# Performance work log

Measured on AMD Instinct MI355X. Metric: run time of the kernel, lower is better.

## Reference

```python
import jax, jax.numpy as jnp
import numpy as np

# --- obs layout constants (from source) ---
OBS_TERM_DIMS = (3, 3, 3, 3, 29, 29, 29, 96)
HISTORY_LEN = 5
BASE_LIN_VEL_DIM = 3
_OFFS = [0]
for d in OBS_TERM_DIMS[:-1]:
    _OFFS.append(_OFFS[-1] + d * HISTORY_LEN)

N = 131072

def _extract_frame(x, frame_idx):
    # proprio frame: 7 terms, 99 dims total
    parts = []
    for t in range(7):
        d = OBS_TERM_DIMS[t]
        s = _OFFS[t] + frame_idx * d
        parts.append(x[:, s:s + d])
    return jnp.concatenate(parts, axis=-1)

def _extract_elevation(x):
    s = _OFFS[7] + (HISTORY_LEN - 1) * OBS_TERM_DIMS[7]
    return x[:, s:s + OBS_TERM_DIMS[7]]  # [N,96]

def setup_inputs() -> dict:
    key = jax.random.key(0)
    ks = jax.random.split(key, 16)
    s = 0.05
    return {
        "x": jax.random.normal(ks[0], (N, 975), jnp.float32),
        "vae_W1": jax.random.normal(ks[1], (480, 256), jnp.float32) * s,
        "vae_b1": jnp.zeros((256,), jnp.float32),
        "vae_Wz": jax.random.normal(ks[2], (256, 32), jnp.float32) * s,
        "vae_bz": jnp.zeros((32,), jnp.float32),
        "vae_Wv": jax.random.normal(ks[3], (256, 3), jnp.float32) * s,
        "vae_bv": jnp.zeros((3,), jnp.float32),
        "ae_W1": jax.random.normal(ks[4], (96, 64), jnp.float32) * s,
        "ae_b1": jnp.zeros((64,), jnp.float32),
        "ae_W2": jax.random.normal(ks[5], (64, 32), jnp.float32) * s,
        "ae_b2": jnp.zeros((32,), jnp.float32),
        "gate_W1": jax.random.normal(ks[6], (32, 64), jnp.float32) * s,
        "gate_b1": jnp.zeros((64,), jnp.float32),
        "gate_W2": jax.random.normal(ks[7], (64, 5), jnp.float32) * s,
        "gate_b2": jnp.zeros((5,), jnp.float32),
        "eW1": jax.random.normal(ks[8], (5, 166, 128), jnp.float32) * s,
        "eb1": jnp.zeros((5, 128), jnp.float32),
        "eW2": jax.random.normal(ks[9], (5, 128, 128), jnp.float32) * s,
        "eb2": jnp.zeros((5, 128), jnp.float32),
        "eW3": jax.random.normal(ks[10], (5, 128, 29), jnp.float32) * s,
        "eb3": jnp.zeros((5, 29), jnp.float32),
    }

def reference(x, vae_W1, vae_b1, vae_Wz, vae_bz, vae_Wv, vae_bv,
              ae_W1, ae_b1, ae_W2, ae_b2,
              gate_W1, gate_b1, gate_W2, gate_b2,
              eW1, eb1, eW2, eb2, eW3, eb3):
    elu = jax.nn.elu
    # feature extraction
    o_t = _extract_frame(x, HISTORY_LEN - 1)                       # [N,99]
    frames = [_extract_frame(x, i)[:, BASE_LIN_VEL_DIM:] for i in range(HISTORY_LEN)]
    vae_hist = jnp.concatenate(frames, axis=-1)                    # [N,480]
    e_t = _extract_elevation(x)                                    # [N,96]
    # VAE estimator (no_grad in original)
    h = elu(vae_hist @ vae_W1 + vae_b1)
    z_H = jax.lax.stop_gradient(h @ vae_Wz + vae_bz)               # [N,32]
    v_pred = jax.lax.stop_gradient(h @ vae_Wv + vae_bv)            # [N,3]
    # AE estimator (no_grad)
    ha = elu(e_t @ ae_W1 + ae_b1)
    z_E = jax.lax.stop_gradient(ha @ ae_W2 + ae_b2)                # [N,32]
    # experts: batched GEMM over 5 experts
    inp = jnp.concatenate([o_t, v_pred, z_H, z_E], axis=-1)        # [N,166]
    h1 = elu(jnp.einsum('ni,eih->neh', inp, eW1) + eb1)            # [N,5,128]
    h2 = elu(jnp.einsum('neh,ehk->nek', h1, eW2) + eb2)            # [N,5,128]
    acts = jnp.einsum('neh,ehk->nek', h2, eW3) + eb3               # [N,5,29]
    # gating
    gl = elu(z_E @ gate_W1 + gate_b1) @ gate_W2 + gate_b2          # [N,5]
    w = jax.nn.softmax(gl, axis=-1)
    return jnp.einsum('ne,nek->nk', w, acts)                       # [N,29]
```

## Files before the change

### kernel.cpp

```cpp
#include <hip/hip_runtime.h>
#include <math.h>

typedef _Float16 f16;
typedef f16  f16x8 __attribute__((ext_vector_type(8)));
typedef float f32x4 __attribute__((ext_vector_type(4)));
typedef unsigned short ushort_t;

#define MFMA16(a, b, c) __builtin_amdgcn_mfma_f32_16x16x32_f16((a), (b), (c), 0, 0, 0)

#define W1T_E 0
#define WZV_E 131072
#define A1T_E 143360
#define A2T_E 149504
#define G1T_E 151552
#define G2T_E 153600
#define E1T_E 154624
#define E2T_E 277504
#define E3T_E 359424
#define F32_B 759808

#define S2_OFF   0
#define B0_OFF   36864
#define H2_OFF   17408
#define ELEV_OFF 62528
#define HA_OFF   62528
#define ZE_OFF   71744
#define WF_OFF   75840
#define SMEM_SZ  77888

__device__ __forceinline__ float elu_f(float v) {
    float e = __expf(v) - 1.f;
    return v > 0.f ? v : e;
}

__device__ __forceinline__ unsigned pk(float a, float b) {
    ushort_t u0 = __builtin_bit_cast(ushort_t, (f16)a);
    ushort_t u1 = __builtin_bit_cast(ushort_t, (f16)b);
    return (unsigned)u0 | ((unsigned)u1 << 16);
}

__device__ __forceinline__ void store4(f16* p, f32x4 v) {
    uint2 t; t.x = pk(v[0], v[1]); t.y = pk(v[2], v[3]);
    *(uint2*)p = t;
}

__device__ __forceinline__ void elu_store4(f16* p, f32x4 v) {
    uint2 t; t.x = pk(elu_f(v[0]), elu_f(v[1])); t.y = pk(elu_f(v[2]), elu_f(v[3]));
    *(uint2*)p = t;
}

__device__ __forceinline__ void sync_lds() {
    asm volatile("s_waitcnt lgkmcnt(0)" ::: "memory");
    __builtin_amdgcn_s_barrier();
    asm volatile("" ::: "memory");
    __builtin_amdgcn_sched_barrier(0);
}

__global__ void prep_kernel(const float* __restrict__ vW1, const float* __restrict__ vWz,
                            const float* __restrict__ vWv, const float* __restrict__ aW1,
                            const float* __restrict__ aW2, const float* __restrict__ gW1,
                            const float* __restrict__ gW2, const float* __restrict__ eW1,
                            const float* __restrict__ eW2, const float* __restrict__ eW3,
                            const float* __restrict__ vbz, const float* __restrict__ vbv,
                            const float* __restrict__ eb3, const float* __restrict__ gb2,
                            char* __restrict__ ws)
{
    int i = blockIdx.x * 256 + threadIdx.x;
    f16* H = (f16*)ws;
    if (i < 131072) {
        int c = i >> 9, ks = i & 511;
        int xcol = 12 + ks;
        float v = 0.f;
        if (xcol >= 15 && xcol <= 494) {
            int hc;
            if (xcol < 60) {
                int t = xcol / 15; int rm = xcol - 15 * t; int f = rm / 3;
                hc = 96 * f + 3 * (t - 1) + (rm - 3 * f);
            } else {
                int t2 = (xcol - 60) / 145; int rm = xcol - 60 - 145 * t2; int f = rm / 29;
                hc = 96 * f + 9 + 29 * t2 + (rm - 29 * f);
            }
            v = vW1[hc * 256 + c];
        }
        H[i] = (f16)v;
    } else if (i < 143360) {
        int j = i - 131072; int c = j / 256, k = j - c * 256;
        float v = (c < 32) ? vWz[k * 32 + c] : ((c < 35) ? vWv[k * 3 + (c - 32)] : 0.f);
        H[i] = (f16)v;
    } else if (i < 149504) {
        int j = i - 143360; int c = j / 96, k = j - c * 96;
        H[i] = (f16)aW1[k * 64 + c];
    } else if (i < 151552) {
        int j = i - 149504; int c = j / 64, k = j - c * 64;
        H[i] = (f16)aW2[k * 32 + c];
    } else if (i < 153600) {
        int j = i - 151552; int c = j / 32, k = j - c * 32;
        H[i] = (f16)gW1[k * 64 + c];
    } else if (i < 154624) {
        int j = i - 153600; int c = j / 64, k = j - c * 64;
        H[i] = (f16)((c < 5) ? gW2[k * 5 + c] : 0.f);
    } else if (i < 277504) {
        int j = i - 154624; int e = j / 24576, jj = j - e * 24576;
        int c = jj / 192, k = jj - c * 192;
        int ko = (k >= 5 && k < 107)   ? (k - 5)
               : (k >= 108 && k < 140) ? (k - 6)
               : (k >= 144 && k < 176) ? (k - 10) : -1;
        H[i] = (f16)((ko >= 0) ? eW1[(e * 166 + ko) * 128 + c] : 0.f);
    } else if (i < 359424) {
        int j = i - 277504; int e = j / 16384, jj = j - e * 16384;
        int c = jj / 128, k = jj - c * 128;
        H[i] = (f16)eW2[(e * 128 + k) * 128 + c];
    } else if (i < 379904) {
        int j = i - 359424; int e = j / 4096, jj = j - e * 4096;
        int c = jj / 128, k = jj - c * 128;
        H[i] = (f16)((c < 29) ? eW3[(e * 128 + k) * 29 + c] : 0.f);
    } else if (i < 380128) {
        int j = i - 379904;
        float* F = (float*)(ws + F32_B);
        float v;
        if (j < 48)       v = (j < 32) ? vbz[j] : ((j < 35) ? vbv[j - 32] : 0.f);
        else if (j < 208) { int t = j - 48; int e = t >> 5, c = t & 31;
                            v = (c < 29) ? eb3[e * 29 + c] : 0.f; }
        else              { int t = j - 208; v = (t < 5) ? gb2[t] : 0.f; }
        F[j] = v;
    }
}

__global__ __launch_bounds__(512, 4) void moe_fused(
    const float* __restrict__ x,
    const float* __restrict__ vb1,
    const float* __restrict__ ab1,
    const float* __restrict__ ab2,
    const float* __restrict__ gb1,
    const float* __restrict__ eb1,
    const float* __restrict__ eb2,
    const char* __restrict__ ws,
    float* __restrict__ out)
{
    __shared__ __align__(16) char smem[SMEM_SZ];
    const int tid  = threadIdx.x;
    const int wv   = tid >> 6;
    const int lane = tid & 63;
    const int lr   = lane & 15;
    const int lg   = lane >> 4;
    const int wh   = wv & 1;
    const int wc   = wv >> 1;
    const int row0 = (int)blockIdx.x * 64;

    const f16* W1T = (const f16*)ws + W1T_E;
    const f16* WZV = (const f16*)ws + WZV_E;
    const f16* A1T = (const f16*)ws + A1T_E;
    const f16* A2T = (const f16*)ws + A2T_E;
    const f16* G1T = (const f16*)ws + G1T_E;
    const f16* G2T = (const f16*)ws + G2T_E;
    const f16* E1T = (const f16*)ws + E1T_E;
    const f16* E2T = (const f16*)ws + E2T_E;
    const f16* E3T = (const f16*)ws + E3T_E;
    const float* BZV  = (const float*)(ws + F32_B);
    const float* EB3P = BZV + 48;
    const float* GB2P = BZV + 208;

    f16* sS2 = (f16*)(smem + S2_OFF);
    f16* sEl = (f16*)(smem + ELEV_OFF);
    f16* sHA = (f16*)(smem + HA_OFF);
    f16* sZE = (f16*)(smem + ZE_OFF);
    f16* sH  = (f16*)(smem + S2_OFF);
    f16* sB0 = (f16*)(smem + B0_OFF);
    f16* sH1 = (f16*)(smem + S2_OFF);
    f16* sH2 = (f16*)(smem + H2_OFF);
    float* sWf = (float*)(smem + WF_OFF);

    {
        if (tid < 16) *(unsigned*)(smem + 62464 + 4 * tid) = 0u;
        const int sr0 = wv * 8;
        for (int rr = 0; rr < 8; ++rr) {
            const int r = sr0 + rr;
            const float* xr = x + (size_t)(row0 + r) * 975;
            if (lane < 48) {
                float a = xr[879 + 2 * lane], b = xr[880 + 2 * lane];
                *(unsigned*)(sEl + r * 104 + 2 * lane) = pk(a, b);
            }
            f16* dst = sS2 + r * 488;
#pragma unroll
            for (int j = 0; j < 4; ++j) {
                int p = j * 64 + lane;
                if (p < 244) {
                    float a = 0.f, b = 0.f;
                    if (p < 242) { a = xr[12 + 2 * p]; b = xr[13 + 2 * p]; }
                    *(unsigned*)(dst + 2 * p) = pk(a, b);
                }
            }
        }
    }
    sync_lds();

    f32x4 g3acc[2];
    {
        f32x4 bi = *(const f32x4*)(ab1 + 16 * wc + 4 * lg);
        g3acc[0] = bi; g3acc[1] = bi;
#pragma unroll
        for (int ks = 0; ks < 3; ++ks) {
            f16x8 wf = *(const f16x8*)(A1T + (16 * wc + lr) * 96 + 32 * ks + 8 * lg);
#pragma unroll
            for (int mm = 0; mm < 2; ++mm) {
                int m = 2 * wh + mm;
                f16x8 bf = *(const f16x8*)(sEl + (16 * m + lr) * 104 + 32 * ks + 8 * lg);
                g3acc[mm] = MFMA16(wf, bf, g3acc[mm]);
            }
        }
    }
    sync_lds();
#pragma unroll
    for (int mm = 0; mm < 2; ++mm)
        elu_store4(sHA + (16 * (2 * wh + mm) + lr) * 72 + 16 * wc + 4 * lg, g3acc[mm]);
    sync_lds();

    if (wv < 4) {
        int c = wv >> 1, h = wv & 1;
        f32x4 bi = *(const f32x4*)(ab2 + 16 * c + 4 * lg);
        f32x4 acc[2]; acc[0] = bi; acc[1] = bi;
#pragma unroll
        for (int ks = 0; ks < 2; ++ks) {
            f16x8 wf = *(const f16x8*)(A2T + (16 * c + lr) * 64 + 32 * ks + 8 * lg);
#pragma unroll
            for (int mm = 0; mm < 2; ++mm) {
                int m = 2 * h + mm;
                f16x8 bf = *(const f16x8*)(sHA + (16 * m + lr) * 72 + 32 * ks + 8 * lg);
                acc[mm] = MFMA16(wf, bf, acc[mm]);
            }
        }
#pragma unroll
        for (int mm = 0; mm < 2; ++mm)
            store4(sZE + (16 * (2 * h + mm) + lr) * 32 + 16 * c + 4 * lg, acc[mm]);
    }
    sync_lds();

    {
        f32x4 bi = *(const f32x4*)(gb1 + 16 * wc + 4 * lg);
        f32x4 acc[2]; acc[0] = bi; acc[1] = bi;
        f16x8 wf = *(const f16x8*)(G1T + (16 * wc + lr) * 32 + 8 * lg);
#pragma unroll
        for (int mm = 0; mm < 2; ++mm) {
            int m = 2 * wh + mm;
            f16x8 bf = *(const f16x8*)(sZE + (16 * m + lr) * 32 + 8 * lg);
            acc[mm] = MFMA16(wf, bf, acc[mm]);
        }
#pragma unroll
        for (int mm = 0; mm < 2; ++mm)
            elu_store4(sHA + (16 * (2 * wh + mm) + lr) * 72 + 16 * wc + 4 * lg, acc[mm]);
    }
    sync_lds();

    if (wv == 0) {
        f32x4 bi = *(const f32x4*)(GB2P + 4 * lg);
        f32x4 acc[4];
#pragma unroll
        for (int m = 0; m < 4; ++m) acc[m] = bi;
#pragma unroll
        for (int ks = 0; ks < 2; ++ks) {
            f16x8 wf = *(const f16x8*)(G2T + lr * 64 + 32 * ks + 8 * lg);
#pragma unroll
            for (int m = 0; m < 4; ++m) {
                f16x8 bf = *(const f16x8*)(sHA + (16 * m + lr) * 72 + 32 * ks + 8 * lg);
                acc[m] = MFMA16(wf, bf, acc[m]);
            }
        }
        if (lg == 0) {
#pragma unroll
            for (int m = 0; m < 4; ++m)
                *(f32x4*)(sWf + (16 * m + lr) * 8) = acc[m];
        } else if (lg == 1) {
#pragma unroll
            for (int m = 0; m < 4; ++m)
                sWf[(16 * m + lr) * 8 + 4] = acc[m][0];
        }
    }
    sync_lds();

    if (tid < 64) {
        float g[5];
#pragma unroll
        for (int e = 0; e < 5; ++e) g[e] = sWf[tid * 8 + e];
        float mx = fmaxf(fmaxf(fmaxf(g[0], g[1]), fmaxf(g[2], g[3])), g[4]);
        float s = 0.f;
#pragma unroll
        for (int e = 0; e < 5; ++e) { g[e] = __expf(g[e] - mx); s += g[e]; }
        float inv = 1.f / s;
#pragma unroll
        for (int e = 0; e < 5; ++e) sWf[tid * 8 + e] = g[e] * inv;
    }

    f32x4 acc1[4][2];
#pragma unroll
    for (int nt = 0; nt < 2; ++nt) {
        f32x4 bi = *(const f32x4*)(vb1 + 32 * wv + 16 * nt + 4 * lg);
#pragma unroll
        for (int m = 0; m < 4; ++m) acc1[m][nt] = bi;
    }
    __builtin_amdgcn_s_setprio(1);
#pragma unroll
    for (int ks = 0; ks < 16; ++ks) {
        f16x8 wf[2];
#pragma unroll
        for (int nt = 0; nt < 2; ++nt)
            wf[nt] = *(const f16x8*)(W1T + (32 * wv + 16 * nt + lr) * 512 + 32 * ks + 8 * lg);
#pragma unroll
        for (int m = 0; m < 4; ++m) {
            f16x8 bf = *(const f16x8*)(sS2 + (16 * m + lr) * 488 + 32 * ks + 8 * lg);
#pragma unroll
            for (int nt = 0; nt < 2; ++nt)
                acc1[m][nt] = MFMA16(wf[nt], bf, acc1[m][nt]);
        }
    }
    __builtin_amdgcn_s_setprio(0);
    const int r_ot = tid >> 3, sub = tid & 7;
    ushort_t otv[13];
#pragma unroll
    for (int i = 0; i < 13; ++i) {
        int j = sub + 8 * i;
        if (j < 99) {
            int s;
            if (j < 3) s = j;
            else if (j < 12) { int jj = j - 3; int t = jj / 3;
                               s = 15 * (t + 1) + (jj - 3 * t); }
            else { int jj = j - 12; int t2 = jj / 29;
                   s = 164 + 145 * t2 + (jj - 29 * t2); }
            otv[i] = __builtin_bit_cast(ushort_t, sS2[r_ot * 488 + s]);
        }
    }
    float we5[5];
    sync_lds();

#pragma unroll
    for (int m = 0; m < 4; ++m)
#pragma unroll
        for (int nt = 0; nt < 2; ++nt)
            elu_store4(sH + (16 * m + lr) * 264 + 32 * wv + 16 * nt + 4 * lg, acc1[m][nt]);
#pragma unroll
    for (int i = 0; i < 13; ++i) {
        int j = sub + 8 * i;
        if (j < 99) sB0[r_ot * 200 + 5 + j] = __builtin_bit_cast(f16, otv[i]);
    }
    {
        char* b0r = (char*)sB0 + r_ot * 400;
        if (sub == 0) { *(uint2*)(b0r + 0) = (uint2){0u, 0u}; *(ushort_t*)(b0r + 8) = 0; }
        else if (sub == 1) { *(uint2*)(b0r + 280) = (uint2){0u, 0u}; }
        else if (sub == 2) { *(uint4*)(b0r + 352) = (uint4){0u,0u,0u,0u}; }
        else if (sub == 3) { *(uint4*)(b0r + 368) = (uint4){0u,0u,0u,0u}; }
    }
    {
        int r = tid >> 3, c4 = tid & 7;
        uint2 v = *(uint2*)((char*)sZE + r * 64 + 8 * c4);
        *(uint2*)((char*)sB0 + r * 400 + 288 + 8 * c4) = v;
    }
#pragma unroll
    for (int e = 0; e < 5; ++e) we5[e] = sWf[(16 * (wv & 3) + lr) * 8 + e];
    sync_lds();

    if (wv < 6) {
        int c = wv >> 1, h = wv & 1;
        f32x4 bz = *(const f32x4*)(BZV + 16 * c + 4 * lg);
        f32x4 acc[2]; acc[0] = bz; acc[1] = bz;
#pragma unroll
        for (int ks = 0; ks < 8; ++ks) {
            f16x8 wf = *(const f16x8*)(WZV + (16 * c + lr) * 256 + 32 * ks + 8 * lg);
#pragma unroll
            for (int mm = 0; mm < 2; ++mm) {
                int m = 2 * h + mm;
                f16x8 bf = *(const f16x8*)(sH + (16 * m + lr) * 264 + 32 * ks + 8 * lg);
                acc[mm] = MFMA16(wf, bf, acc[mm]);
            }
        }
        if (c < 2 || lg == 0) {
            int col = (c < 2) ? (108 + 16 * c + 4 * lg) : 104;
#pragma unroll
            for (int mm = 0; mm < 2; ++mm)
                store4(sB0 + (16 * (2 * h + mm) + lr) * 200 + col, acc[mm]);
        }
    }
    sync_lds();

    f32x4 oacc = (f32x4)0.f;
    const int mrow = wv & 3;
    const int nt3  = wv >> 2;

    for (int e = 0; e < 5; ++e) {
        {
            f32x4 bi = *(const f32x4*)(eb1 + e * 128 + 16 * wv + 4 * lg);
            f32x4 acc[4];
#pragma unroll
            for (int m = 0; m < 4; ++m) acc[m] = bi;
            __builtin_amdgcn_s_setprio(1);
#pragma unroll
            for (int ks = 0; ks < 6; ++ks) {
                f16x8 wf = *(const f16x8*)(E1T + (e * 128 + 16 * wv + lr) * 192 + 32 * ks + 8 * lg);
#pragma unroll
                for (int m = 0; m < 4; ++m) {
                    f16x8 bf = *(const f16x8*)(sB0 + (16 * m + lr) * 200 + 32 * ks + 8 * lg);
                    acc[m] = MFMA16(wf, bf, acc[m]);
                }
            }
            __builtin_amdgcn_s_setprio(0);
#pragma unroll
            for (int m = 0; m < 4; ++m)
                elu_store4(sH1 + (16 * m + lr) * 136 + 16 * wv + 4 * lg, acc[m]);
        }
        sync_lds();
        {
            f32x4 bi = *(const f32x4*)(eb2 + e * 128 + 16 * wv + 4 * lg);
            f32x4 acc[4];
#pragma unroll
            for (int m = 0; m < 4; ++m) acc[m] = bi;
            __builtin_amdgcn_s_setprio(1);
#pragma unroll
            for (int ks = 0; ks < 4; ++ks) {
                f16x8 wf = *(const f16x8*)(E2T + (e * 128 + 16 * wv + lr) * 128 + 32 * ks + 8 * lg);
#pragma unroll
                for (int m = 0; m < 4; ++m) {
                    f16x8 bf = *(const f16x8*)(sH1 + (16 * m + lr) * 136 + 32 * ks + 8 * lg);
                    acc[m] = MFMA16(wf, bf, acc[m]);
                }
            }
            __builtin_amdgcn_s_setprio(0);
#pragma unroll
            for (int m = 0; m < 4; ++m)
                elu_store4(sH2 + (16 * m + lr) * 136 + 16 * wv + 4 * lg, acc[m]);
        }
        sync_lds();
        {
            f32x4 a3 = *(const f32x4*)(EB3P + e * 32 + 16 * nt3 + 4 * lg);
#pragma unroll
            for (int ks = 0; ks < 4; ++ks) {
                f16x8 bf = *(const f16x8*)(sH2 + (16 * mrow + lr) * 136 + 32 * ks + 8 * lg);
                f16x8 wf = *(const f16x8*)(E3T + (e * 32 + 16 * nt3 + lr) * 128 + 32 * ks + 8 * lg);
                a3 = MFMA16(wf, bf, a3);
            }
            float we = we5[e];
#pragma unroll
            for (int r = 0; r < 4; ++r) oacc[r] += we * a3[r];
        }
        sync_lds();
    }

    {
        int row = row0 + 16 * mrow + lr;
#pragma unroll
        for (int r = 0; r < 4; ++r) {
            int col = 16 * nt3 + 4 * lg + r;
            if (col < 29) out[(size_t)row * 29 + col] = oacc[r];
        }
    }
}

extern "C" void kernel_launch(void* const* d_in, const int* in_sizes, int n_in,
                              void* d_out, int out_size, void* d_ws, size_t ws_size,
                              hipStream_t stream)
{
    (void)n_in; (void)out_size; (void)ws_size;
    const float* x   = (const float*)d_in[0];
    const float* vW1 = (const float*)d_in[1];
    const float* vb1 = (const float*)d_in[2];
    const float* vWz = (const float*)d_in[3];
    const float* vbz = (const float*)d_in[4];
    const float* vWv = (const float*)d_in[5];
    const float* vbv = (const float*)d_in[6];
    const float* aW1 = (const float*)d_in[7];
    const float* ab1 = (const float*)d_in[8];
    const float* aW2 = (const float*)d_in[9];
    const float* ab2 = (const float*)d_in[10];
    const float* gW1 = (const float*)d_in[11];
    const float* gb1 = (const float*)d_in[12];
    const float* gW2 = (const float*)d_in[13];
    const float* gb2 = (const float*)d_in[14];
    const float* eW1 = (const float*)d_in[15];
    const float* eb1 = (const float*)d_in[16];
    const float* eW2 = (const float*)d_in[17];
    const float* eb2 = (const float*)d_in[18];
    const float* eW3 = (const float*)d_in[19];
    const float* eb3 = (const float*)d_in[20];

    int n = in_sizes[0] / 975;

    prep_kernel<<<(380128 + 255) / 256, 256, 0, stream>>>(
        vW1, vWz, vWv, aW1, aW2, gW1, gW2, eW1, eW2, eW3, vbz, vbv, eb3, gb2, (char*)d_ws);

    moe_fused<<<n / 64, 512, 0, stream>>>(
        x, vb1, ab1, ab2, gb1, eb1, eb2, (const char*)d_ws, (float*)d_out);
}
```

Before: 298.7 us.

## Split fused MoE kernel into front-end and 128-row expert kernels via workspace

The single fused kernel is split in two. The first kernel computes the VAE, AE and gating front-end and writes the 166-wide expert input and the softmax weights to global workspace. The second kernel processes 128 rows per block for the expert MLPs, so each wave loads its expert weight fragments once and reuses them across 8 row tiles instead of 4. In exchange it adds a global write and read of roughly 400 bytes per row, a second launch, and a larger LDS footprint per block.

```diff
diff --git a/kernel.cpp b/kernel.cpp
--- a/kernel.cpp
+++ b/kernel.cpp
@@ -18,15 +18,22 @@
 #define E2T_E 277504
 #define E3T_E 359424
 #define F32_B 759808
+#define INP_B 1048576
+#define W5_B  53477376
 
 #define S2_OFF   0
 #define B0_OFF   36864
-#define H2_OFF   17408
 #define ELEV_OFF 62528
 #define HA_OFF   62528
 #define ZE_OFF   71744
 #define WF_OFF   75840
 #define SMEM_SZ  77888
+
+#define IL_OFF   0
+#define BH1_OFF  51200
+#define BH2_OFF  86016
+#define BW5_OFF  120832
+#define BSMEM    124928
 
 __device__ __forceinline__ float elu_f(float v) {
     float e = __expf(v) - 1.f;
@@ -126,16 +133,13 @@
     }
 }
 
-__global__ __launch_bounds__(512, 4) void moe_fused(
+__global__ __launch_bounds__(512, 2) void moe_front(
     const float* __restrict__ x,
     const float* __restrict__ vb1,
     const float* __restrict__ ab1,
     const float* __restrict__ ab2,
     const float* __restrict__ gb1,
-    const float* __restrict__ eb1,
-    const float* __restrict__ eb2,
-    const char* __restrict__ ws,
-    float* __restrict__ out)
+    char* __restrict__ ws)
 {
     __shared__ __align__(16) char smem[SMEM_SZ];
     const int tid  = threadIdx.x;
@@ -143,8 +147,8 @@
     const int lane = tid & 63;
     const int lr   = lane & 15;
     const int lg   = lane >> 4;
-    const int wh   = wv & 1;
-    const int wc   = wv >> 1;
+    const int rh   = wv & 1;
+    const int cq   = wv >> 1;
     const int row0 = (int)blockIdx.x * 64;
 
     const f16* W1T = (const f16*)ws + W1T_E;
@@ -153,11 +157,7 @@
     const f16* A2T = (const f16*)ws + A2T_E;
     const f16* G1T = (const f16*)ws + G1T_E;
     const f16* G2T = (const f16*)ws + G2T_E;
-    const f16* E1T = (const f16*)ws + E1T_E;
-    const f16* E2T = (const f16*)ws + E2T_E;
-    const f16* E3T = (const f16*)ws + E3T_E;
     const float* BZV  = (const float*)(ws + F32_B);
-    const float* EB3P = BZV + 48;
     const float* GB2P = BZV + 208;
 
     f16* sS2 = (f16*)(smem + S2_OFF);
@@ -166,8 +166,6 @@
     f16* sZE = (f16*)(smem + ZE_OFF);
     f16* sH  = (f16*)(smem + S2_OFF);
     f16* sB0 = (f16*)(smem + B0_OFF);
-    f16* sH1 = (f16*)(smem + S2_OFF);
-    f16* sH2 = (f16*)(smem + H2_OFF);
     float* sWf = (float*)(smem + WF_OFF);
 
     {
@@ -196,14 +194,14 @@
 
     f32x4 g3acc[2];
     {
-        f32x4 bi = *(const f32x4*)(ab1 + 16 * wc + 4 * lg);
+        f32x4 bi = *(const f32x4*)(ab1 + 16 * cq + 4 * lg);
         g3acc[0] = bi; g3acc[1] = bi;
 #pragma unroll
         for (int ks = 0; ks < 3; ++ks) {
-            f16x8 wf = *(const f16x8*)(A1T + (16 * wc + lr) * 96 + 32 * ks + 8 * lg);
+            f16x8 wf = *(const f16x8*)(A1T + (16 * cq + lr) * 96 + 32 * ks + 8 * lg);
 #pragma unroll
             for (int mm = 0; mm < 2; ++mm) {
-                int m = 2 * wh + mm;
+                int m = 2 * rh + mm;
                 f16x8 bf = *(const f16x8*)(sEl + (16 * m + lr) * 104 + 32 * ks + 8 * lg);
                 g3acc[mm] = MFMA16(wf, bf, g3acc[mm]);
             }
@@ -212,7 +210,7 @@
     sync_lds();
 #pragma unroll
     for (int mm = 0; mm < 2; ++mm)
-        elu_store4(sHA + (16 * (2 * wh + mm) + lr) * 72 + 16 * wc + 4 * lg, g3acc[mm]);
+        elu_store4(sHA + (16 * (2 * rh + mm) + lr) * 72 + 16 * cq + 4 * lg, g3acc[mm]);
     sync_lds();
 
     if (wv < 4) {
@@ -236,18 +234,18 @@
     sync_lds();
 
     {
-        f32x4 bi = *(const f32x4*)(gb1 + 16 * wc + 4 * lg);
+        f32x4 bi = *(const f32x4*)(gb1 + 16 * cq + 4 * lg);
         f32x4 acc[2]; acc[0] = bi; acc[1] = bi;
-        f16x8 wf = *(const f16x8*)(G1T + (16 * wc + lr) * 32 + 8 * lg);
+        f16x8 wf = *(const f16x8*)(G1T + (16 * cq + lr) * 32 + 8 * lg);
 #pragma unroll
         for (int mm = 0; mm < 2; ++mm) {
-            int m = 2 * wh + mm;
+            int m = 2 * rh + mm;
             f16x8 bf = *(const f16x8*)(sZE + (16 * m + lr) * 32 + 8 * lg);
             acc[mm] = MFMA16(wf, bf, acc[mm]);
         }
 #pragma unroll
         for (int mm = 0; mm < 2; ++mm)
-            elu_store4(sHA + (16 * (2 * wh + mm) + lr) * 72 + 16 * wc + 4 * lg, acc[mm]);
+            elu_store4(sHA + (16 * (2 * rh + mm) + lr) * 72 + 16 * cq + 4 * lg, acc[mm]);
     }
     sync_lds();
 
@@ -288,6 +286,7 @@
         float inv = 1.f / s;
 #pragma unroll
         for (int e = 0; e < 5; ++e) sWf[tid * 8 + e] = g[e] * inv;
+        sWf[tid * 8 + 5] = 0.f; sWf[tid * 8 + 6] = 0.f; sWf[tid * 8 + 7] = 0.f;
     }
 
     f32x4 acc1[4][2];
@@ -328,7 +327,6 @@
             otv[i] = __builtin_bit_cast(ushort_t, sS2[r_ot * 488 + s]);
         }
     }
-    float we5[5];
     sync_lds();
 
 #pragma unroll
@@ -353,8 +351,6 @@
         uint2 v = *(uint2*)((char*)sZE + r * 64 + 8 * c4);
         *(uint2*)((char*)sB0 + r * 400 + 288 + 8 * c4) = v;
     }
-#pragma unroll
-    for (int e = 0; e < 5; ++e) we5[e] = sWf[(16 * (wv & 3) + lr) * 8 + e];
     sync_lds();
 
     if (wv < 6) {
@@ -380,75 +376,136 @@
     }
     sync_lds();
 
-    f32x4 oacc = (f32x4)0.f;
-    const int mrow = wv & 3;
-    const int nt3  = wv >> 2;
+    {
+        const uint4* srcB = (const uint4*)sB0;
+        uint4* dstB = (uint4*)(ws + INP_B + (size_t)row0 * 400);
+#pragma unroll
+        for (int it = 0; it < 4; ++it) {
+            int idx = it * 512 + tid;
+            if (idx < 1600) dstB[idx] = srcB[idx];
+        }
+        const uint4* srcW = (const uint4*)sWf;
+        uint4* dstW = (uint4*)(ws + W5_B + (size_t)row0 * 32);
+        if (tid < 128) dstW[tid] = srcW[tid];
+    }
+}
+
+__global__ __launch_bounds__(512, 2) void moe_experts(
+    const char* __restrict__ ws,
+    const float* __restrict__ eb1,
+    const float* __restrict__ eb2,
+    float* __restrict__ out)
+{
+    __shared__ __align__(16) char smem[BSMEM];
+    const int tid  = threadIdx.x;
+    const int wv   = tid >> 6;
+    const int lane = tid & 63;
+    const int lr   = lane & 15;
+    const int lg   = lane >> 4;
+    const int row0 = (int)blockIdx.x * 128;
+
+    const f16* E1T = (const f16*)ws + E1T_E;
+    const f16* E2T = (const f16*)ws + E2T_E;
+    const f16* E3T = (const f16*)ws + E3T_E;
+    const float* EB3P = (const float*)(ws + F32_B) + 48;
+
+    f16* IL = (f16*)(smem + IL_OFF);
+    f16* H1 = (f16*)(smem + BH1_OFF);
+    f16* H2 = (f16*)(smem + BH2_OFF);
+    float* W5 = (float*)(smem + BW5_OFF);
+
+    {
+        const uint4* srcB = (const uint4*)(ws + INP_B + (size_t)row0 * 400);
+#pragma unroll
+        for (int it = 0; it < 7; ++it) {
+            int idx = it * 512 + tid;
+            if (idx < 3200) ((uint4*)IL)[idx] = srcB[idx];
+        }
+        const uint4* srcW = (const uint4*)(ws + W5_B + (size_t)row0 * 32);
+        if (tid < 256) ((uint4*)W5)[tid] = srcW[tid];
+    }
+    __syncthreads();
+
+    float we5[5];
+#pragma unroll
+    for (int e = 0; e < 5; ++e) we5[e] = W5[(16 * wv + lr) * 8 + e];
+
+    f32x4 oacc[2]; oacc[0] = (f32x4)0.f; oacc[1] = (f32x4)0.f;
 
     for (int e = 0; e < 5; ++e) {
         {
             f32x4 bi = *(const f32x4*)(eb1 + e * 128 + 16 * wv + 4 * lg);
-            f32x4 acc[4];
-#pragma unroll
-            for (int m = 0; m < 4; ++m) acc[m] = bi;
+            f32x4 acc[8];
+#pragma unroll
+            for (int m = 0; m < 8; ++m) acc[m] = bi;
             __builtin_amdgcn_s_setprio(1);
 #pragma unroll
             for (int ks = 0; ks < 6; ++ks) {
                 f16x8 wf = *(const f16x8*)(E1T + (e * 128 + 16 * wv + lr) * 192 + 32 * ks + 8 * lg);
 #pragma unroll
-                for (int m = 0; m < 4; ++m) {
-                    f16x8 bf = *(const f16x8*)(sB0 + (16 * m + lr) * 200 + 32 * ks + 8 * lg);
+                for (int m = 0; m < 8; ++m) {
+                    f16x8 bf = *(const f16x8*)(IL + (16 * m + lr) * 200 + 32 * ks + 8 * lg);
                     acc[m] = MFMA16(wf, bf, acc[m]);
                 }
             }
             __builtin_amdgcn_s_setprio(0);
 #pragma unroll
-            for (int m = 0; m < 4; ++m)
-                elu_store4(sH1 + (16 * m + lr) * 136 + 16 * wv + 4 * lg, acc[m]);
-        }
-        sync_lds();
+            for (int m = 0; m < 8; ++m)
+                elu_store4(H1 + (16 * m + lr) * 136 + 16 * wv + 4 * lg, acc[m]);
+        }
+        __syncthreads();
         {
             f32x4 bi = *(const f32x4*)(eb2 + e * 128 + 16 * wv + 4 * lg);
-            f32x4 acc[4];
-#pragma unroll
-            for (int m = 0; m < 4; ++m) acc[m] = bi;
+            f32x4 acc[8];
+#pragma unroll
+            for (int m = 0; m < 8; ++m) acc[m] = bi;
             __builtin_amdgcn_s_setprio(1);
 #pragma unroll
             for (int ks = 0; ks < 4; ++ks) {
                 f16x8 wf = *(const f16x8*)(E2T + (e * 128 + 16 * wv + lr) * 128 + 32 * ks + 8 * lg);
 #pragma unroll
-                for (int m = 0; m < 4; ++m) {
-                    f16x8 bf = *(const f16x8*)(sH1 + (16 * m + lr) * 136 + 32 * ks + 8 * lg);
+                for (int m = 0; m < 8; ++m) {
+                    f16x8 bf = *(const f16x8*)(H1 + (16 * m + lr) * 136 + 32 * ks + 8 * lg);
                     acc[m] = MFMA16(wf, bf, acc[m]);
                 }
             }
             __builtin_amdgcn_s_setprio(0);
 #pragma unroll
-            for (int m = 0; m < 4; ++m)
-                elu_store4(sH2 + (16 * m + lr) * 136 + 16 * wv + 4 * lg, acc[m]);
-        }
-        sync_lds();
+            for (int m = 0; m < 8; ++m)
+                elu_store4(H2 + (16 * m + lr) * 136 + 16 * wv + 4 * lg, acc[m]);
+        }
+        __syncthreads();
         {
-            f32x4 a3 = *(const f32x4*)(EB3P + e * 32 + 16 * nt3 + 4 * lg);
+            f32x4 a3[2];
+#pragma unroll
+            for (int ct = 0; ct < 2; ++ct)
+                a3[ct] = *(const f32x4*)(EB3P + e * 32 + 16 * ct + 4 * lg);
 #pragma unroll
             for (int ks = 0; ks < 4; ++ks) {
-                f16x8 bf = *(const f16x8*)(sH2 + (16 * mrow + lr) * 136 + 32 * ks + 8 * lg);
-                f16x8 wf = *(const f16x8*)(E3T + (e * 32 + 16 * nt3 + lr) * 128 + 32 * ks + 8 * lg);
-                a3 = MFMA16(wf, bf, a3);
+                f16x8 bf = *(const f16x8*)(H2 + (16 * wv + lr) * 136 + 32 * ks + 8 * lg);
+#pragma unroll
+                for (int ct = 0; ct < 2; ++ct) {
+                    f16x8 wf = *(const f16x8*)(E3T + (e * 32 + 16 * ct + lr) * 128 + 32 * ks + 8 * lg);
+                    a3[ct] = MFMA16(wf, bf, a3[ct]);
+                }
             }
             float we = we5[e];
 #pragma unroll
-            for (int r = 0; r < 4; ++r) oacc[r] += we * a3[r];
-        }
-        sync_lds();
-    }
-
-    {
-        int row = row0 + 16 * mrow + lr;
-#pragma unroll
-        for (int r = 0; r < 4; ++r) {
-            int col = 16 * nt3 + 4 * lg + r;
-            if (col < 29) out[(size_t)row * 29 + col] = oacc[r];
-        }
+            for (int ct = 0; ct < 2; ++ct)
+#pragma unroll
+                for (int r = 0; r < 4; ++r) oacc[ct][r] += we * a3[ct][r];
+        }
+    }
+
+    {
+        int row = row0 + 16 * wv + lr;
+#pragma unroll
+        for (int ct = 0; ct < 2; ++ct)
+#pragma unroll
+            for (int r = 0; r < 4; ++r) {
+                int col = 16 * ct + 4 * lg + r;
+                if (col < 29) out[(size_t)row * 29 + col] = oacc[ct][r];
+            }
     }
 }
 
@@ -484,6 +541,9 @@
     prep_kernel<<<(380128 + 255) / 256, 256, 0, stream>>>(
         vW1, vWz, vWv, aW1, aW2, gW1, gW2, eW1, eW2, eW3, vbz, vbv, eb3, gb2, (char*)d_ws);
 
-    moe_fused<<<n / 64, 512, 0, stream>>>(
-        x, vb1, ab1, ab2, gb1, eb1, eb2, (const char*)d_ws, (float*)d_out);
-}
+    moe_front<<<n / 64, 512, 0, stream>>>(
+        x, vb1, ab1, ab2, gb1, (char*)d_ws);
+
+    moe_experts<<<n / 128, 512, 0, stream>>>(
+        (const char*)d_ws, eb1, eb2, (float*)d_out);
+}
```

Measured after the change: 314.8 us. 1.05x slower.
